# Performance work log

Measured on AMD Instinct MI355X. Metric: run time of the kernel, lower is better.

Reference implementation:

```python
import jax, jax.numpy as jnp
import numpy as np

B, DIM, RES = 32, 384, 28
KEY_DIM, HEADS, RATIO = 32, 8, 4
D = RATIO * KEY_DIM            # 128 value dim per head
DH = D * HEADS                 # 1024
NHKD = KEY_DIM * HEADS         # 256
H_QKV = DH + 2 * NHKD          # 1536
N = RES * RES                  # 784 tokens
EPS = 1e-5
SCALE = KEY_DIM ** -0.5


def _bias_idxs():
    pts = [(i, j) for i in range(RES) for j in range(RES)]
    offs, idxs = {}, []
    for p1 in pts:
        for p2 in pts:
            o = (abs(p1[0] - p2[0]), abs(p1[1] - p2[1]))
            if o not in offs:
                offs[o] = len(offs)
            idxs.append(offs[o])
    return np.asarray(idxs, np.int32).reshape(N, N), len(offs)


def hardswish(x):
    return x * jnp.clip(x + 3.0, 0.0, 6.0) * (1.0 / 6.0)


def bn_eval(x, g, b, m, v):
    # inference-mode BatchNorm2d over channel axis 1
    s = (g / jnp.sqrt(v + EPS))[None, :, None, None]
    return (x - m[None, :, None, None]) * s + b[None, :, None, None]


def setup_inputs() -> dict:
    key = jax.random.key(0)
    ks = jax.random.split(key, 12)
    idxs, n_off = _bias_idxs()
    return {
        "x": jax.random.normal(ks[0], (B, DIM, RES, RES), jnp.float32),
        "qkv_w": jax.random.normal(ks[1], (H_QKV, DIM), jnp.float32) * 0.02,
        "qkv_g": jax.random.uniform(ks[2], (H_QKV,), jnp.float32, 0.5, 1.5),
        "qkv_b": jax.random.normal(ks[3], (H_QKV,), jnp.float32) * 0.1,
        "qkv_m": jax.random.normal(ks[4], (H_QKV,), jnp.float32) * 0.1,
        "qkv_v": jax.random.uniform(ks[5], (H_QKV,), jnp.float32, 0.5, 1.5),
        "attn_biases": jax.random.normal(ks[6], (HEADS, n_off), jnp.float32) * 0.02,
        "proj_w": jax.random.normal(ks[7], (DIM, DH), jnp.float32) * 0.02,
        "proj_g": jax.random.uniform(ks[8], (DIM,), jnp.float32, 0.5, 1.5),
        "proj_b": jax.random.normal(ks[9], (DIM,), jnp.float32) * 0.1,
        "proj_m": jax.random.normal(ks[10], (DIM,), jnp.float32) * 0.1,
        "proj_v": jax.random.uniform(ks[11], (DIM,), jnp.float32, 0.5, 1.5),
        "bias_idxs": jnp.asarray(idxs),
    }


def reference(x, qkv_w, qkv_g, qkv_b, qkv_m, qkv_v, attn_biases,
              proj_w, proj_g, proj_b, proj_m, proj_v, bias_idxs):
    Bb, C, Hh, Ww = x.shape
    n = Hh * Ww
    # qkv: 1x1 conv + BN + hardswish
    y = jnp.einsum('bchw,oc->bohw', x, qkv_w)
    y = hardswish(bn_eval(y, qkv_g, qkv_b, qkv_m, qkv_v))
    y = y.reshape(Bb, HEADS, H_QKV // HEADS, n)
    q, k, v = jnp.split(y, [KEY_DIM, 2 * KEY_DIM], axis=2)  # [B,h,kd,N] x2, [B,h,d,N]
    bias = attn_biases[:, bias_idxs]                         # [heads, N, N]
    attn = jnp.einsum('bhkn,bhkm->bhnm', q, k) * SCALE + bias[None]
    attn = jax.nn.softmax(attn, axis=-1)
    out = jnp.einsum('bhdm,bhnm->bhdn', v, attn)             # v @ attn^T
    out = out.reshape(Bb, DH, Hh, Ww)
    # proj: hardswish -> 1x1 conv + BN + hardswish
    out = hardswish(out)
    out = jnp.einsum('bchw,oc->bohw', out, proj_w)
    out = hardswish(bn_eval(out, proj_g, proj_b, proj_m, proj_v))
    return out
```

## Files before the change

### kernel.cpp

```cpp
#include <hip/hip_runtime.h>
#include <cstdint>

constexpr int BATCH = 32;
constexpr int DIMC  = 384;
constexpr int NTOK  = 784;
constexpr int KD    = 32;
constexpr int DV    = 128;
constexpr int PERH  = 192;
constexpr int HQKV  = 1536;
constexpr int DHTOT = 1024;
constexpr int NMC   = 25;
constexpr int VPB   = NMC * 8 * 512;
constexpr float BNEPS  = 1e-5f;
constexpr float LOG2E  = 1.4426950408889634f;
constexpr float QSCL2  = 0.17677669529663687f * LOG2E;

#define DEVFN static __device__ __forceinline__

using f16x8 = __attribute__((ext_vector_type(8))) _Float16;
using f32x4 = __attribute__((ext_vector_type(4))) float;

DEVFN float hswish(float x) {
  float t = fminf(fmaxf(x + 3.0f, 0.0f), 6.0f);
  return x * t * (1.0f / 6.0f);
}
DEVFN uint16_t f2h(float f) { return __builtin_bit_cast(uint16_t, (_Float16)f); }
DEVFN float h2f(uint16_t u) { return (float)__builtin_bit_cast(_Float16, u); }
DEVFN uint32_t pk2h(float a, float b) {
  return __builtin_bit_cast(uint32_t, __builtin_amdgcn_cvt_pkrtz(a, b));
}

DEVFN void gload16(const void* g, void* l) {
  __builtin_amdgcn_global_load_lds(
      (const __attribute__((address_space(1))) void*)g,
      (__attribute__((address_space(3))) void*)l, 16, 0, 0);
}

__global__ __launch_bounds__(256) void convert_w(
    const float* __restrict__ qw, const float* __restrict__ pw,
    uint16_t* __restrict__ qwh, uint16_t* __restrict__ pwh)
{
  constexpr int QW4 = (HQKV * DIMC) / 4;
  constexpr int PW4 = (DIMC * DHTOT) / 4;
  int idx = blockIdx.x * 256 + threadIdx.x;
  if (idx < QW4) {
    float4 v = reinterpret_cast<const float4*>(qw)[idx];
    uint2 p;
    p.x = pk2h(v.x, v.y);
    p.y = pk2h(v.z, v.w);
    reinterpret_cast<uint2*>(qwh)[idx] = p;
  } else if (idx < QW4 + PW4) {
    int i2 = idx - QW4;
    float4 v = reinterpret_cast<const float4*>(pw)[i2];
    uint2 p;
    p.x = pk2h(v.x, v.y);
    p.y = pk2h(v.z, v.w);
    reinterpret_cast<uint2*>(pwh)[i2] = p;
  }
}

__global__ __launch_bounds__(256) void bias_build(
    const float* __restrict__ biases, uint16_t* __restrict__ biasH)
{
  const int n = blockIdx.x, h = blockIdx.y;
  const int t = threadIdx.x;
  if (t >= 196) return;
  const int m0 = 4*t;
  const int ri = (n * 2341) >> 16;
  const int rj = n - ri*28;
  const float* bh_ = biases + (size_t)h * NTOK;
  uint16_t o[4];
  #pragma unroll
  for (int r = 0; r < 4; ++r) {
    int m  = m0 + r;
    int im = (m * 2341) >> 16;
    int jm = m - im*28;
    int di = ri - im; di = di < 0 ? -di : di;
    int dj = rj - jm; dj = dj < 0 ? -dj : dj;
    o[r] = f2h(bh_[di*28 + dj] * LOG2E);
  }
  uint2 p;
  p.x = (uint32_t)o[0] | ((uint32_t)o[1] << 16);
  p.y = (uint32_t)o[2] | ((uint32_t)o[3] << 16);
  *reinterpret_cast<uint2*>(biasH + ((size_t)h*NTOK + n)*NTOK + m0) = p;
}

__global__ __launch_bounds__(256) void transpose_x(
    const float* __restrict__ x, uint16_t* __restrict__ xT)
{
  const int b = blockIdx.z, n0 = blockIdx.x * 32, c0 = blockIdx.y * 32;
  __shared__ float t[32][33];
  const int tx = threadIdx.x & 31, ty = threadIdx.x >> 5;
  const float* xb = x + (size_t)b * DIMC * NTOK;
  #pragma unroll
  for (int k = 0; k < 4; ++k) {
    int c = c0 + ty + 8*k;
    int n = n0 + tx;
    t[ty + 8*k][tx] = (n < NTOK) ? xb[(size_t)c * NTOK + n] : 0.f;
  }
  __syncthreads();
  uint16_t* xTb = xT + (size_t)b * NTOK * DIMC;
  #pragma unroll
  for (int k = 0; k < 4; ++k) {
    int n = n0 + ty + 8*k;
    if (n < NTOK) xTb[(size_t)n * DIMC + c0 + tx] = f2h(t[tx][ty + 8*k]);
  }
}

__global__ __launch_bounds__(256) void qkv_gemm(
    const uint16_t* __restrict__ wh, const uint16_t* __restrict__ xT,
    const float* __restrict__ gw, const float* __restrict__ bw,
    const float* __restrict__ mw, const float* __restrict__ vw,
    uint16_t* __restrict__ qb, uint16_t* __restrict__ kb, uint16_t* __restrict__ vb)
{
  const int b  = blockIdx.z;
  const int m0 = blockIdx.y * 128;
  const int n0 = blockIdx.x * 64;
  __shared__ __align__(16) uint16_t As[2][128*64];
  __shared__ __align__(16) uint16_t Bs[2][64*64];

  const int tid = threadIdx.x;
  const int w = tid >> 6, l = tid & 63, lg = l >> 4, ln = l & 15;
  const int wr = w >> 1, wc = w & 1;
  const int wbase = tid & 192;
  const uint16_t* xb = xT + (size_t)b * NTOK * DIMC;

  f32x4 acc[4][2];
  #pragma unroll
  for (int mi = 0; mi < 4; ++mi)
    #pragma unroll
    for (int ni = 0; ni < 2; ++ni) acc[mi][ni] = (f32x4){0.f,0.f,0.f,0.f};

  auto stage = [&](int buf, int k0) {
    #pragma unroll
    for (int j = 0; j < 4; ++j) {
      int s = j*256 + tid;
      int row = s >> 3, sl = s & 7;
      int srck = k0 + 8 * (sl ^ (row & 7));
      gload16(wh + (size_t)(m0 + row) * DIMC + srck,
              &As[buf][(j*256 + wbase) * 8]);
    }
    #pragma unroll
    for (int j = 0; j < 2; ++j) {
      int s = j*256 + tid;
      int row = s >> 3, sl = s & 7;
      int nrow = n0 + row; if (nrow > NTOK-1) nrow = NTOK-1;
      int srck = k0 + 8 * (sl ^ (row & 7));
      gload16(xb + (size_t)nrow * DIMC + srck,
              &Bs[buf][(j*256 + wbase) * 8]);
    }
  };

  stage(0, 0);
  int cur = 0;
  for (int k0 = 0; k0 < DIMC; k0 += 64) {
    __syncthreads();
    if (k0 + 64 < DIMC) stage(cur ^ 1, k0 + 64);
    #pragma unroll
    for (int kk = 0; kk < 2; ++kk) {
      f16x8 af[4], bf[2];
      #pragma unroll
      for (int mi = 0; mi < 4; ++mi) {
        int row = 64*wr + 16*mi + ln;
        int slot = (4*kk + lg) ^ (row & 7);
        af[mi] = *reinterpret_cast<const f16x8*>(&As[cur][row*64 + slot*8]);
      }
      #pragma unroll
      for (int ni = 0; ni < 2; ++ni) {
        int row = 32*wc + 16*ni + ln;
        int slot = (4*kk + lg) ^ (row & 7);
        bf[ni] = *reinterpret_cast<const f16x8*>(&Bs[cur][row*64 + slot*8]);
      }
      #pragma unroll
      for (int mi = 0; mi < 4; ++mi)
        #pragma unroll
        for (int ni = 0; ni < 2; ++ni)
          acc[mi][ni] = __builtin_amdgcn_mfma_f32_16x16x32_f16(
              af[mi], bf[ni], acc[mi][ni], 0, 0, 0);
    }
    cur ^= 1;
  }

  #pragma unroll
  for (int mi = 0; mi < 4; ++mi) {
    const int ob = m0 + 64*wr + 16*mi;
    const int h  = ob / PERH;
    const int r0 = ob - h * PERH;
    const int bh = b*8 + h;
    float sc[4], sh[4];
    #pragma unroll
    for (int r = 0; r < 4; ++r) {
      int o = ob + 4*lg + r;
      float s = gw[o] * rsqrtf(vw[o] + BNEPS);
      sc[r] = s; sh[r] = bw[o] - mw[o]*s;
    }
    #pragma unroll
    for (int ni = 0; ni < 2; ++ni) {
      int n = n0 + 32*wc + 16*ni + ln;
      if (n >= NTOK) continue;
      float v4[4];
      #pragma unroll
      for (int r = 0; r < 4; ++r) v4[r] = hswish(acc[mi][ni][r]*sc[r] + sh[r]);
      if (r0 < 2*KD) {
        if (r0 < KD) {
          #pragma unroll
          for (int r = 0; r < 4; ++r) v4[r] *= QSCL2;
        }
        uint16_t* base = (r0 < KD) ? qb : kb;
        int dd = (r0 & 16) + 4*lg;
        uint2 p;
        p.x = pk2h(v4[0], v4[1]);
        p.y = pk2h(v4[2], v4[3]);
        *reinterpret_cast<uint2*>(base + ((size_t)bh*NTOK + n)*KD + dd) = p;
      } else {
        const int dv0 = r0 - 2*KD;
        const int mc = n >> 5, mm = n & 31;
        const int lgv = mm >> 3, jj = mm & 7;
        uint16_t* vblk = vb + (size_t)bh*VPB + ((size_t)mc*8)*512 + lgv*128 + jj;
        #pragma unroll
        for (int r = 0; r < 4; ++r) {
          int dv = dv0 + 4*lg + r;
          int dt = dv >> 4, lnv = dv & 15;
          vblk[(size_t)dt*512 + lnv*8] = f2h(v4[r]);
        }
      }
    }
  }
}

__global__ __launch_bounds__(256) void attn_kernel(
    const uint16_t* __restrict__ Qb, const uint16_t* __restrict__ Kb,
    const uint16_t* __restrict__ Vb, const uint16_t* __restrict__ biasH,
    uint16_t* __restrict__ a2T)
{
  const int bh = blockIdx.x;
  const int b_ = bh >> 3;
  const int h  = bh & 7;

  __shared__ __align__(16) uint16_t plds[4][2][16][72];

  const int tid = threadIdx.x;
  const int w   = tid >> 6;
  const int l   = tid & 63;
  const int lg  = l >> 4;
  const int ln  = l & 15;

  const int tile = blockIdx.y * 4 + w;
  if (tile >= 25) return;
  const int n0 = tile * 32;
  const int nA = n0 + ln;
  int nBr = n0 + 16 + ln;
  const int nB = (nBr < NTOK) ? nBr : (NTOK-1);

  const uint16_t* Kbase = Kb + (size_t)bh * NTOK * KD;
  const uint16_t* Vbase = Vb + (size_t)bh * VPB;
  const uint16_t* browA = biasH + ((size_t)h * NTOK + nA) * NTOK;
  const uint16_t* browB = biasH + ((size_t)h * NTOK + nB) * NTOK;

  const f16x8 qfA = *reinterpret_cast<const f16x8*>(
      Qb + ((size_t)bh*NTOK + nA)*KD + 8*lg);
  const f16x8 qfB = *reinterpret_cast<const f16x8*>(
      Qb + ((size_t)bh*NTOK + nB)*KD + 8*lg);

  float MA = -1e30f, LA = 0.f, MB = -1e30f, LB = 0.f;
  f32x4 accA[8], accB[8];
  #pragma unroll
  for (int dt = 0; dt < 8; ++dt) {
    accA[dt] = (f32x4){0.f,0.f,0.f,0.f};
    accB[dt] = (f32x4){0.f,0.f,0.f,0.f};
  }

  f16x8 kf[4];
  uint2  ba[4], bb[4];
  auto loadKB = [&](int mbase) {
    #pragma unroll
    for (int t = 0; t < 4; ++t) {
      int mrow = mbase + 16*t + ln; if (mrow > NTOK-1) mrow = NTOK-1;
      kf[t] = *reinterpret_cast<const f16x8*>(Kbase + (size_t)mrow*KD + 8*lg);
      int mo = mbase + 16*t + 4*lg; if (mo > NTOK-4) mo = NTOK-4;
      ba[t] = *reinterpret_cast<const uint2*>(browA + mo);
      bb[t] = *reinterpret_cast<const uint2*>(browB + mo);
    }
  };
  loadKB(0);

  for (int mb = 0; mb < NTOK; mb += 64) {
    const int rem   = (NTOK - mb) >> 4;
    const int ntile = rem < 4 ? rem : 4;
    const int mc0   = mb >> 5;

    float pA[16], pB[16];
    #pragma unroll
    for (int i = 0; i < 16; ++i) { pA[i] = -1e30f; pB[i] = -1e30f; }

    #pragma unroll
    for (int t = 0; t < 4; ++t) {
      if (t < ntile) {
        f32x4 cA, cB;
        cA[0] = h2f((uint16_t)(ba[t].x & 0xffffu)); cA[1] = h2f((uint16_t)(ba[t].x >> 16));
        cA[2] = h2f((uint16_t)(ba[t].y & 0xffffu)); cA[3] = h2f((uint16_t)(ba[t].y >> 16));
        cB[0] = h2f((uint16_t)(bb[t].x & 0xffffu)); cB[1] = h2f((uint16_t)(bb[t].x >> 16));
        cB[2] = h2f((uint16_t)(bb[t].y & 0xffffu)); cB[3] = h2f((uint16_t)(bb[t].y >> 16));
        f32x4 sA = __builtin_amdgcn_mfma_f32_16x16x32_f16(kf[t], qfA, cA, 0, 0, 0);
        f32x4 sB = __builtin_amdgcn_mfma_f32_16x16x32_f16(kf[t], qfB, cB, 0, 0, 0);
        #pragma unroll
        for (int r = 0; r < 4; ++r) { pA[4*t+r] = sA[r]; pB[4*t+r] = sB[r]; }
      }
    }

    if (mb + 64 < NTOK) loadKB(mb + 64);

    f16x8 vf0[8];
    #pragma unroll
    for (int dt = 0; dt < 8; ++dt)
      vf0[dt] = *reinterpret_cast<const f16x8*>(
          Vbase + ((size_t)mc0*8 + dt)*512 + l*8);

    float mA01, mB01;
    {
      float a0 = fmaxf(pA[0], pA[1]),  a1 = fmaxf(pA[2], pA[3]);
      float a2 = fmaxf(pA[4], pA[5]),  a3 = fmaxf(pA[6], pA[7]);
      float a4 = fmaxf(pA[8], pA[9]),  a5 = fmaxf(pA[10], pA[11]);
      float a6 = fmaxf(pA[12], pA[13]), a7 = fmaxf(pA[14], pA[15]);
      mA01 = fmaxf(fmaxf(fmaxf(a0,a1), fmaxf(a2,a3)), fmaxf(fmaxf(a4,a5), fmaxf(a6,a7)));
      float b0 = fmaxf(pB[0], pB[1]),  b1 = fmaxf(pB[2], pB[3]);
      float b2 = fmaxf(pB[4], pB[5]),  b3 = fmaxf(pB[6], pB[7]);
      float b4 = fmaxf(pB[8], pB[9]),  b5 = fmaxf(pB[10], pB[11]);
      float b6 = fmaxf(pB[12], pB[13]), b7 = fmaxf(pB[14], pB[15]);
      mB01 = fmaxf(fmaxf(fmaxf(b0,b1), fmaxf(b2,b3)), fmaxf(fmaxf(b4,b5), fmaxf(b6,b7)));
    }
    float mxA = fmaxf(mA01, __shfl_xor(mA01, 16)); mxA = fmaxf(mxA, __shfl_xor(mxA, 32));
    float mxB = fmaxf(mB01, __shfl_xor(mB01, 16)); mxB = fmaxf(mxB, __shfl_xor(mxB, 32));

    float MnA = fmaxf(MA, mxA), MnB = fmaxf(MB, mxB);

    if (!__all((mxA <= MA) & (mxB <= MB))) {
      float alA = exp2f(MA - MnA), alB = exp2f(MB - MnB);
      LA *= alA; LB *= alB;
      float alA4[4], alB4[4];
      #pragma unroll
      for (int r = 0; r < 4; ++r) {
        alA4[r] = __shfl(alA, 20*lg + r);
        alB4[r] = __shfl(alB, 20*lg + r);
      }
      #pragma unroll
      for (int dt = 0; dt < 8; ++dt) {
        #pragma unroll
        for (int r = 0; r < 4; ++r) { accA[dt][r] *= alA4[r]; accB[dt][r] *= alB4[r]; }
      }
    }
    MA = MnA; MB = MnB;

    float sumA, sumB;
    {
      #pragma unroll
      for (int i = 0; i < 16; ++i) {
        pA[i] = exp2f(pA[i] - MnA);
        pB[i] = exp2f(pB[i] - MnB);
      }
      float s0 = (pA[0]+pA[1]) + (pA[2]+pA[3]);
      float s1 = (pA[4]+pA[5]) + (pA[6]+pA[7]);
      float s2 = (pA[8]+pA[9]) + (pA[10]+pA[11]);
      float s3 = (pA[12]+pA[13]) + (pA[14]+pA[15]);
      sumA = (s0+s1) + (s2+s3);
      float t0 = (pB[0]+pB[1]) + (pB[2]+pB[3]);
      float t1 = (pB[4]+pB[5]) + (pB[6]+pB[7]);
      float t2 = (pB[8]+pB[9]) + (pB[10]+pB[11]);
      float t3 = (pB[12]+pB[13]) + (pB[14]+pB[15]);
      sumB = (t0+t1) + (t2+t3);
    }
    sumA += __shfl_xor(sumA, 16); sumA += __shfl_xor(sumA, 32);
    sumB += __shfl_xor(sumB, 16); sumB += __shfl_xor(sumB, 32);
    LA += sumA; LB += sumB;

    #pragma unroll
    for (int t = 0; t < 4; ++t) {
      uint2 ka, kb2;
      ka.x  = pk2h(pA[4*t+0], pA[4*t+1]);
      ka.y  = pk2h(pA[4*t+2], pA[4*t+3]);
      kb2.x = pk2h(pB[4*t+0], pB[4*t+1]);
      kb2.y = pk2h(pB[4*t+2], pB[4*t+3]);
      *reinterpret_cast<uint2*>(&plds[w][0][ln][16*t + 4*lg]) = ka;
      *reinterpret_cast<uint2*>(&plds[w][1][ln][16*t + 4*lg]) = kb2;
    }

    {
      f16x8 pfA = *reinterpret_cast<const f16x8*>(&plds[w][0][ln][8*lg]);
      f16x8 pfB = *reinterpret_cast<const f16x8*>(&plds[w][1][ln][8*lg]);
      __builtin_amdgcn_s_setprio(1);
      #pragma unroll
      for (int dt = 0; dt < 8; ++dt) {
        accA[dt] = __builtin_amdgcn_mfma_f32_16x16x32_f16(pfA, vf0[dt], accA[dt], 0, 0, 0);
        accB[dt] = __builtin_amdgcn_mfma_f32_16x16x32_f16(pfB, vf0[dt], accB[dt], 0, 0, 0);
      }
      __builtin_amdgcn_s_setprio(0);
    }

    if (mb + 32 < NTOK) {
      f16x8 pfA = *reinterpret_cast<const f16x8*>(&plds[w][0][ln][32 + 8*lg]);
      f16x8 pfB = *reinterpret_cast<const f16x8*>(&plds[w][1][ln][32 + 8*lg]);
      f16x8 vf1[8];
      #pragma unroll
      for (int dt = 0; dt < 8; ++dt)
        vf1[dt] = *reinterpret_cast<const f16x8*>(
            Vbase + ((size_t)(mc0+1)*8 + dt)*512 + l*8);
      __builtin_amdgcn_s_setprio(1);
      #pragma unroll
      for (int dt = 0; dt < 8; ++dt) {
        accA[dt] = __builtin_amdgcn_mfma_f32_16x16x32_f16(pfA, vf1[dt], accA[dt], 0, 0, 0);
        accB[dt] = __builtin_amdgcn_mfma_f32_16x16x32_f16(pfB, vf1[dt], accB[dt], 0, 0, 0);
      }
      __builtin_amdgcn_s_setprio(0);
    }
  }

  float liA = 1.0f / LA, liB = 1.0f / LB;
  float liA4[4], liB4[4];
  #pragma unroll
  for (int r = 0; r < 4; ++r) {
    liA4[r] = __shfl(liA, 20*lg + r);
    liB4[r] = __shfl(liB, 20*lg + r);
  }
  #pragma unroll
  for (int r = 0; r < 4; ++r) {
    int rowA = n0 + 4*lg + r;
    #pragma unroll
    for (int dt = 0; dt < 8; ++dt)
      a2T[((size_t)b_*NTOK + rowA)*DHTOT + h*DV + 16*dt + ln] =
          f2h(hswish(accA[dt][r] * liA4[r]));
    int rowB = n0 + 16 + 4*lg + r;
    if (rowB < NTOK) {
      #pragma unroll
      for (int dt = 0; dt < 8; ++dt)
        a2T[((size_t)b_*NTOK + rowB)*DHTOT + h*DV + 16*dt + ln] =
            f2h(hswish(accB[dt][r] * liB4[r]));
    }
  }
}

__global__ __launch_bounds__(256) void proj_gemm(
    const uint16_t* __restrict__ wh, const uint16_t* __restrict__ a2T,
    const float* __restrict__ gw, const float* __restrict__ bw,
    const float* __restrict__ mw, const float* __restrict__ vw,
    float* __restrict__ out)
{
  const int b  = blockIdx.z;
  const int m0 = blockIdx.y * 128;
  const int n0 = blockIdx.x * 64;
  __shared__ __align__(16) uint16_t As[2][128*64];
  __shared__ __align__(16) uint16_t Bs[2][64*64];

  const int tid = threadIdx.x;
  const int w = tid >> 6, l = tid & 63, lg = l >> 4, ln = l & 15;
  const int wr = w >> 1, wc = w & 1;
  const int wbase = tid & 192;
  const uint16_t* ab = a2T + (size_t)b * NTOK * DHTOT;

  f32x4 acc[4][2];
  #pragma unroll
  for (int mi = 0; mi < 4; ++mi)
    #pragma unroll
    for (int ni = 0; ni < 2; ++ni) acc[mi][ni] = (f32x4){0.f,0.f,0.f,0.f};

  auto stage = [&](int buf, int k0) {
    #pragma unroll
    for (int j = 0; j < 4; ++j) {
      int s = j*256 + tid;
      int row = s >> 3, sl = s & 7;
      int srck = k0 + 8 * (sl ^ (row & 7));
      gload16(wh + (size_t)(m0 + row) * DHTOT + srck,
              &As[buf][(j*256 + wbase) * 8]);
    }
    #pragma unroll
    for (int j = 0; j < 2; ++j) {
      int s = j*256 + tid;
      int row = s >> 3, sl = s & 7;
      int nrow = n0 + row; if (nrow > NTOK-1) nrow = NTOK-1;
      int srck = k0 + 8 * (sl ^ (row & 7));
      gload16(ab + (size_t)nrow * DHTOT + srck,
              &Bs[buf][(j*256 + wbase) * 8]);
    }
  };

  stage(0, 0);
  int cur = 0;
  for (int k0 = 0; k0 < DHTOT; k0 += 64) {
    __syncthreads();
    if (k0 + 64 < DHTOT) stage(cur ^ 1, k0 + 64);
    #pragma unroll
    for (int kk = 0; kk < 2; ++kk) {
      f16x8 af[4], bf[2];
      #pragma unroll
      for (int mi = 0; mi < 4; ++mi) {
        int row = 64*wr + 16*mi + ln;
        int slot = (4*kk + lg) ^ (row & 7);
        af[mi] = *reinterpret_cast<const f16x8*>(&As[cur][row*64 + slot*8]);
      }
      #pragma unroll
      for (int ni = 0; ni < 2; ++ni) {
        int row = 32*wc + 16*ni + ln;
        int slot = (4*kk + lg) ^ (row & 7);
        bf[ni] = *reinterpret_cast<const f16x8*>(&Bs[cur][row*64 + slot*8]);
      }
      #pragma unroll
      for (int mi = 0; mi < 4; ++mi)
        #pragma unroll
        for (int ni = 0; ni < 2; ++ni)
          acc[mi][ni] = __builtin_amdgcn_mfma_f32_16x16x32_f16(
              af[mi], bf[ni], acc[mi][ni], 0, 0, 0);
    }
    cur ^= 1;
  }

  #pragma unroll
  for (int mi = 0; mi < 4; ++mi) {
    float sc[4], sh[4];
    #pragma unroll
    for (int r = 0; r < 4; ++r) {
      int o = m0 + 64*wr + 16*mi + 4*lg + r;
      float s = gw[o] * rsqrtf(vw[o] + BNEPS);
      sc[r] = s; sh[r] = bw[o] - mw[o]*s;
    }
    #pragma unroll
    for (int ni = 0; ni < 2; ++ni) {
      int n = n0 + 32*wc + 16*ni + ln;
      if (n >= NTOK) continue;
      #pragma unroll
      for (int r = 0; r < 4; ++r) {
        int o = m0 + 64*wr + 16*mi + 4*lg + r;
        out[((size_t)b*DIMC + o)*NTOK + n] = hswish(acc[mi][ni][r]*sc[r] + sh[r]);
      }
    }
  }
}

extern "C" void kernel_launch(void* const* d_in, const int* in_sizes, int n_in,
                              void* d_out, int out_size, void* d_ws, size_t ws_size,
                              hipStream_t stream)
{
  const float* x  = (const float*)d_in[0];
  const float* qw = (const float*)d_in[1];
  const float* qg = (const float*)d_in[2];
  const float* qb_ = (const float*)d_in[3];
  const float* qm = (const float*)d_in[4];
  const float* qv = (const float*)d_in[5];
  const float* ab = (const float*)d_in[6];
  const float* pw = (const float*)d_in[7];
  const float* pg = (const float*)d_in[8];
  const float* pb = (const float*)d_in[9];
  const float* pm = (const float*)d_in[10];
  const float* pv = (const float*)d_in[11];
  float* out = (float*)d_out;

  uint16_t* qwh   = (uint16_t*)d_ws;
  uint16_t* pwh   = qwh + (size_t)HQKV * DIMC;
  uint16_t* biasH = pwh + (size_t)DIMC * DHTOT;
  uint16_t* dyn   = biasH + (size_t)8 * NTOK * NTOK;
  const size_t fixed_bytes =
      ((size_t)HQKV*DIMC + (size_t)DIMC*DHTOT + (size_t)8*NTOK*NTOK) * 2;

  const size_t XT_B = (size_t)NTOK * DIMC;
  const size_t QK_B = (size_t)8 * NTOK * KD;
  const size_t V_B  = (size_t)8 * VPB;
  const size_t A2_B = (size_t)NTOK * DHTOT;
  const size_t PER_B = XT_B + 2*QK_B + V_B + A2_B;

  size_t avail = (ws_size > fixed_bytes) ? (ws_size - fixed_bytes) : 0;
  int nb = (int)(avail / (PER_B * 2));
  if (nb > BATCH) nb = BATCH;
  if (nb < 1) nb = 1;

  uint16_t* xTb  = dyn;
  uint16_t* qbuf = xTb  + (size_t)nb * XT_B;
  uint16_t* kbuf = qbuf + (size_t)nb * QK_B;
  uint16_t* vbuf = kbuf + (size_t)nb * QK_B;
  uint16_t* a2   = vbuf + (size_t)nb * V_B;

  convert_w<<<960, 256, 0, stream>>>(qw, pw, qwh, pwh);
  bias_build<<<dim3(NTOK, 8), 256, 0, stream>>>(ab, biasH);

  for (int b0 = 0; b0 < BATCH; b0 += nb) {
    int cb = BATCH - b0; if (cb > nb) cb = nb;
    const float* xb = x + (size_t)b0 * DIMC * NTOK;
    float* ob = out + (size_t)b0 * DIMC * NTOK;

    transpose_x<<<dim3(25, 12, cb), 256, 0, stream>>>(xb, xTb);
    qkv_gemm<<<dim3(13, 12, cb), 256, 0, stream>>>(qwh, xTb, qg, qb_, qm, qv,
                                                   qbuf, kbuf, vbuf);
    attn_kernel<<<dim3(cb * 8, 7), 256, 0, stream>>>(qbuf, kbuf, vbuf, biasH, a2);
    proj_gemm<<<dim3(13, 3, cb), 256, 0, stream>>>(pwh, a2, pg, pb, pm, pv, ob);
  }
}
```

Measured before the change: 350.7 us.

## Stage V tiles into double-buffered LDS shared across waves in attention kernel

```diff
diff --git a/kernel.cpp b/kernel.cpp
--- a/kernel.cpp
+++ b/kernel.cpp
@@ -237,6 +237,7 @@
   const int b_ = bh >> 3;
   const int h  = bh & 7;
 
+  __shared__ __align__(16) uint16_t vl[2][16*512];
   __shared__ __align__(16) uint16_t plds[4][2][16][72];
 
   const int tid = threadIdx.x;
@@ -245,8 +246,9 @@
   const int lg  = l >> 4;
   const int ln  = l & 15;
 
-  const int tile = blockIdx.y * 4 + w;
-  if (tile >= 25) return;
+  const int tile0 = blockIdx.y * 4 + w;
+  const bool act  = tile0 < 25;
+  const int tile  = act ? tile0 : 24;
   const int n0 = tile * 32;
   const int nA = n0 + ln;
   int nBr = n0 + 16 + ln;
@@ -270,24 +272,26 @@
     accB[dt] = (f32x4){0.f,0.f,0.f,0.f};
   }
 
-  f16x8 kf[4];
-  uint2  ba[4], bb[4];
-  auto loadKB = [&](int mbase) {
-    #pragma unroll
-    for (int t = 0; t < 4; ++t) {
-      int mrow = mbase + 16*t + ln; if (mrow > NTOK-1) mrow = NTOK-1;
-      kf[t] = *reinterpret_cast<const f16x8*>(Kbase + (size_t)mrow*KD + 8*lg);
-      int mo = mbase + 16*t + 4*lg; if (mo > NTOK-4) mo = NTOK-4;
-      ba[t] = *reinterpret_cast<const uint2*>(browA + mo);
-      bb[t] = *reinterpret_cast<const uint2*>(browB + mo);
+  auto stageV = [&](int buf, int mc0) {
+    #pragma unroll
+    for (int j = 0; j < 4; ++j) {
+      int blk = w*4 + j;
+      int mc = mc0 + (blk >> 3); if (mc > NMC-1) mc = NMC-1;
+      int dt = blk & 7;
+      gload16(Vbase + ((size_t)mc*8 + dt)*512 + l*8,
+              &vl[buf][blk*512]);
     }
   };
-  loadKB(0);
+
+  stageV(0, 0);
+  int cur = 0;
 
   for (int mb = 0; mb < NTOK; mb += 64) {
+    __syncthreads();
+    if (mb + 64 < NTOK) stageV(cur ^ 1, (mb + 64) >> 5);
+
     const int rem   = (NTOK - mb) >> 4;
     const int ntile = rem < 4 ? rem : 4;
-    const int mc0   = mb >> 5;
 
     float pA[16], pB[16];
     #pragma unroll
@@ -296,25 +300,21 @@
     #pragma unroll
     for (int t = 0; t < 4; ++t) {
       if (t < ntile) {
+        f16x8 kf = *reinterpret_cast<const f16x8*>(
+            Kbase + (size_t)(mb + 16*t + ln)*KD + 8*lg);
+        uint2 ba = *reinterpret_cast<const uint2*>(browA + mb + 16*t + 4*lg);
+        uint2 bb = *reinterpret_cast<const uint2*>(browB + mb + 16*t + 4*lg);
         f32x4 cA, cB;
-        cA[0] = h2f((uint16_t)(ba[t].x & 0xffffu)); cA[1] = h2f((uint16_t)(ba[t].x >> 16));
-        cA[2] = h2f((uint16_t)(ba[t].y & 0xffffu)); cA[3] = h2f((uint16_t)(ba[t].y >> 16));
-        cB[0] = h2f((uint16_t)(bb[t].x & 0xffffu)); cB[1] = h2f((uint16_t)(bb[t].x >> 16));
-        cB[2] = h2f((uint16_t)(bb[t].y & 0xffffu)); cB[3] = h2f((uint16_t)(bb[t].y >> 16));
-        f32x4 sA = __builtin_amdgcn_mfma_f32_16x16x32_f16(kf[t], qfA, cA, 0, 0, 0);
-        f32x4 sB = __builtin_amdgcn_mfma_f32_16x16x32_f16(kf[t], qfB, cB, 0, 0, 0);
+        cA[0] = h2f((uint16_t)(ba.x & 0xffffu)); cA[1] = h2f((uint16_t)(ba.x >> 16));
+        cA[2] = h2f((uint16_t)(ba.y & 0xffffu)); cA[3] = h2f((uint16_t)(ba.y >> 16));
+        cB[0] = h2f((uint16_t)(bb.x & 0xffffu)); cB[1] = h2f((uint16_t)(bb.x >> 16));
+        cB[2] = h2f((uint16_t)(bb.y & 0xffffu)); cB[3] = h2f((uint16_t)(bb.y >> 16));
+        f32x4 sA = __builtin_amdgcn_mfma_f32_16x16x32_f16(kf, qfA, cA, 0, 0, 0);
+        f32x4 sB = __builtin_amdgcn_mfma_f32_16x16x32_f16(kf, qfB, cB, 0, 0, 0);
         #pragma unroll
         for (int r = 0; r < 4; ++r) { pA[4*t+r] = sA[r]; pB[4*t+r] = sB[r]; }
       }
     }
-
-    if (mb + 64 < NTOK) loadKB(mb + 64);
-
-    f16x8 vf0[8];
-    #pragma unroll
-    for (int dt = 0; dt < 8; ++dt)
-      vf0[dt] = *reinterpret_cast<const f16x8*>(
-          Vbase + ((size_t)mc0*8 + dt)*512 + l*8);
 
     float mA01, mB01;
     {
@@ -333,24 +333,7 @@
     float mxB = fmaxf(mB01, __shfl_xor(mB01, 16)); mxB = fmaxf(mxB, __shfl_xor(mxB, 32));
 
     float MnA = fmaxf(MA, mxA), MnB = fmaxf(MB, mxB);
-
-    if (!__all((mxA <= MA) & (mxB <= MB))) {
-      float alA = exp2f(MA - MnA), alB = exp2f(MB - MnB);
-      LA *= alA; LB *= alB;
-      float alA4[4], alB4[4];
-      #pragma unroll
-      for (int r = 0; r < 4; ++r) {
-        alA4[r] = __shfl(alA, 20*lg + r);
-        alB4[r] = __shfl(alB, 20*lg + r);
-      }
-      #pragma unroll
-      for (int dt = 0; dt < 8; ++dt) {
-        #pragma unroll
-        for (int r = 0; r < 4; ++r) { accA[dt][r] *= alA4[r]; accB[dt][r] *= alB4[r]; }
-      }
-    }
-    MA = MnA; MB = MnB;
-
+    float alA = exp2f(MA - MnA), alB = exp2f(MB - MnB);
     float sumA, sumB;
     {
       #pragma unroll
@@ -371,7 +354,20 @@
     }
     sumA += __shfl_xor(sumA, 16); sumA += __shfl_xor(sumA, 32);
     sumB += __shfl_xor(sumB, 16); sumB += __shfl_xor(sumB, 32);
-    LA += sumA; LB += sumB;
+    LA = LA * alA + sumA; MA = MnA;
+    LB = LB * alB + sumB; MB = MnB;
+
+    float alA4[4], alB4[4];
+    #pragma unroll
+    for (int r = 0; r < 4; ++r) {
+      alA4[r] = __shfl(alA, 20*lg + r);
+      alB4[r] = __shfl(alB, 20*lg + r);
+    }
+    #pragma unroll
+    for (int dt = 0; dt < 8; ++dt) {
+      #pragma unroll
+      for (int r = 0; r < 4; ++r) { accA[dt][r] *= alA4[r]; accB[dt][r] *= alB4[r]; }
+    }
 
     #pragma unroll
     for (int t = 0; t < 4; ++t) {
@@ -390,8 +386,9 @@
       __builtin_amdgcn_s_setprio(1);
       #pragma unroll
       for (int dt = 0; dt < 8; ++dt) {
-        accA[dt] = __builtin_amdgcn_mfma_f32_16x16x32_f16(pfA, vf0[dt], accA[dt], 0, 0, 0);
-        accB[dt] = __builtin_amdgcn_mfma_f32_16x16x32_f16(pfB, vf0[dt], accB[dt], 0, 0, 0);
+        f16x8 vf = *reinterpret_cast<const f16x8*>(&vl[cur][dt*512 + l*8]);
+        accA[dt] = __builtin_amdgcn_mfma_f32_16x16x32_f16(pfA, vf, accA[dt], 0, 0, 0);
+        accB[dt] = __builtin_amdgcn_mfma_f32_16x16x32_f16(pfB, vf, accB[dt], 0, 0, 0);
       }
       __builtin_amdgcn_s_setprio(0);
     }
@@ -399,41 +396,40 @@
     if (mb + 32 < NTOK) {
       f16x8 pfA = *reinterpret_cast<const f16x8*>(&plds[w][0][ln][32 + 8*lg]);
       f16x8 pfB = *reinterpret_cast<const f16x8*>(&plds[w][1][ln][32 + 8*lg]);
-      f16x8 vf1[8];
+      __builtin_amdgcn_s_setprio(1);
+      #pragma unroll
+      for (int dt = 0; dt < 8; ++dt) {
+        f16x8 vf = *reinterpret_cast<const f16x8*>(&vl[cur][(8+dt)*512 + l*8]);
+        accA[dt] = __builtin_amdgcn_mfma_f32_16x16x32_f16(pfA, vf, accA[dt], 0, 0, 0);
+        accB[dt] = __builtin_amdgcn_mfma_f32_16x16x32_f16(pfB, vf, accB[dt], 0, 0, 0);
+      }
+      __builtin_amdgcn_s_setprio(0);
+    }
+    cur ^= 1;
+  }
+
+  if (act) {
+    float liA = 1.0f / LA, liB = 1.0f / LB;
+    float liA4[4], liB4[4];
+    #pragma unroll
+    for (int r = 0; r < 4; ++r) {
+      liA4[r] = __shfl(liA, 20*lg + r);
+      liB4[r] = __shfl(liB, 20*lg + r);
+    }
+    #pragma unroll
+    for (int r = 0; r < 4; ++r) {
+      int rowA = n0 + 4*lg + r;
       #pragma unroll
       for (int dt = 0; dt < 8; ++dt)
-        vf1[dt] = *reinterpret_cast<const f16x8*>(
-            Vbase + ((size_t)(mc0+1)*8 + dt)*512 + l*8);
-      __builtin_amdgcn_s_setprio(1);
-      #pragma unroll
-      for (int dt = 0; dt < 8; ++dt) {
-        accA[dt] = __builtin_amdgcn_mfma_f32_16x16x32_f16(pfA, vf1[dt], accA[dt], 0, 0, 0);
-        accB[dt] = __builtin_amdgcn_mfma_f32_16x16x32_f16(pfB, vf1[dt], accB[dt], 0, 0, 0);
-      }
-      __builtin_amdgcn_s_setprio(0);
-    }
-  }
-
-  float liA = 1.0f / LA, liB = 1.0f / LB;
-  float liA4[4], liB4[4];
-  #pragma unroll
-  for (int r = 0; r < 4; ++r) {
-    liA4[r] = __shfl(liA, 20*lg + r);
-    liB4[r] = __shfl(liB, 20*lg + r);
-  }
-  #pragma unroll
-  for (int r = 0; r < 4; ++r) {
-    int rowA = n0 + 4*lg + r;
-    #pragma unroll
-    for (int dt = 0; dt < 8; ++dt)
-      a2T[((size_t)b_*NTOK + rowA)*DHTOT + h*DV + 16*dt + ln] =
-          f2h(hswish(accA[dt][r] * liA4[r]));
-    int rowB = n0 + 16 + 4*lg + r;
-    if (rowB < NTOK) {
-      #pragma unroll
-      for (int dt = 0; dt < 8; ++dt)
-        a2T[((size_t)b_*NTOK + rowB)*DHTOT + h*DV + 16*dt + ln] =
-            f2h(hswish(accB[dt][r] * liB4[r]));
+        a2T[((size_t)b_*NTOK + rowA)*DHTOT + h*DV + 16*dt + ln] =
+            f2h(hswish(accA[dt][r] * liA4[r]));
+      int rowB = n0 + 16 + 4*lg + r;
+      if (rowB < NTOK) {
+        #pragma unroll
+        for (int dt = 0; dt < 8; ++dt)
+          a2T[((size_t)b_*NTOK + rowB)*DHTOT + h*DV + 16*dt + ln] =
+              f2h(hswish(accB[dt][r] * liB4[r]));
+      }
     }
   }
 }
```

Measured after the change: 333.2 us. -5.0%, faster.
